# Performance work log

Hardware: AMD Instinct MI355X
Metric: run time of the kernel (lower is better)

The kernel has to match this reference:

```python
import jax, jax.numpy as jnp
import numpy as np

# ---- module hyper-params (match init_kwargs) ----
B, C_IN, C_OUT, K, H, W = 16, 128, 128, 3, 56, 56
M, G, STRIDE, RED = 2, 2, 1, 16
R = max(RED, C_IN // RED)            # GC_Attention bottleneck width = 16
MO = M * C_OUT                       # gc_att output channels
GROUPS = G * C_OUT                   # grouped 1x1 fc groups = 256
IN_PG = MO // GROUPS                 # in channels per group = M // G = 1
COUT_FC = C_OUT * C_IN * K * K       # generated weight elements per sample
OUT_PG = COUT_FC // GROUPS           # out channels per group = 576
PAD = K // 2
LN_EPS = 1e-5


def setup_inputs() -> dict:
    key = jax.random.key(0)
    ks = jax.random.split(key, 6)
    sc = 0.05
    return {
        "x": jax.random.normal(ks[0], (B, C_IN, H, W), jnp.float32),
        # GC_Attention: conv_mask (1x1, C->1)
        "w_mask": jax.random.normal(ks[1], (C_IN,), jnp.float32) * sc,
        "b_mask": jnp.zeros((), jnp.float32),
        # transform: conv1x1 C->R, LayerNorm(R), ReLU, conv1x1 R->M*out
        "w1": jax.random.normal(ks[2], (R, C_IN), jnp.float32) * sc,
        "b1": jnp.zeros((R,), jnp.float32),
        "ln_g": jnp.ones((R,), jnp.float32),
        "ln_b": jnp.zeros((R,), jnp.float32),
        "w2": jax.random.normal(ks[3], (MO, R), jnp.float32) * sc,
        "b2": jnp.zeros((MO,), jnp.float32),
        # fc: grouped 1x1 conv, groups=G*out, stored [groups, out_pg, in_pg]
        "w_fc": jax.random.normal(ks[4], (GROUPS, OUT_PG, IN_PG), jnp.float32) * sc,
        "b_fc": jnp.zeros((COUT_FC,), jnp.float32),
    }


def reference(x, w_mask, b_mask, w1, b1, ln_g, ln_b, w2, b2, w_fc, b_fc):
    b, c, h, w = x.shape
    # --- GC_Attention: global-context pooling via spatial softmax ---
    mask = jnp.einsum('bchw,c->bhw', x, w_mask) + b_mask        # [b,h,w]
    att = jax.nn.softmax(mask.reshape(b, -1), axis=-1)          # [b,hw]
    ctx = jnp.einsum('bcs,bs->bc', x.reshape(b, c, -1), att)    # [b,C]
    # bottleneck transform (1x1 convs on [b,*,1,1] == dense layers)
    t = ctx @ w1.T + b1                                          # [b,R]
    mu = t.mean(-1, keepdims=True)
    var = t.var(-1, keepdims=True)
    t = (t - mu) / jnp.sqrt(var + LN_EPS) * ln_g + ln_b          # LayerNorm over R
    t = jax.nn.relu(t)
    a = jax.nn.sigmoid(t @ w2.T + b2)                            # [b, M*out]
    # --- grouped 1x1 conv: generate per-sample conv weights ---
    xw = jnp.einsum('bgi,goi->bgo', a.reshape(b, GROUPS, IN_PG), w_fc)
    xw = xw.reshape(b, COUT_FC) + b_fc
    Wd = xw.reshape(b, C_OUT, C_IN, K, K)                        # per-sample kernels
    # --- per-sample conv2d (torch: groups=b on batch-folded input) ---
    def conv1(xi, wi):
        return jax.lax.conv_general_dilated(
            xi[None], wi, (STRIDE, STRIDE), [(PAD, PAD), (PAD, PAD)],
            dimension_numbers=('NCHW', 'OIHW', 'NCHW'))[0]
    return jax.vmap(conv1)(x, Wd)                                # [b, out, H, W]
```

## Files before the change

### kernel.cpp

```cpp
#include <hip/hip_runtime.h>
#include <hip/hip_bf16.h>
#include <math.h>

#define BATCH 16
#define CIN   128
#define COUT  128
#define SS    3136
#define KKTOT 1152
#define XT_ROW 8192
#define XT_PER_B (58*XT_ROW)
#define NKB   18

typedef __attribute__((ext_vector_type(8))) __bf16 bf16x8;
typedef __attribute__((ext_vector_type(4))) float  floatx4;

static __device__ __forceinline__ unsigned short f2bf(float f) {
  union { float f; unsigned u; } v; v.f = f;
  unsigned r = v.u + 0x7fffu + ((v.u >> 16) & 1u);
  return (unsigned short)(r >> 16);
}
static __device__ __forceinline__ float bf2f(unsigned short u) {
  union { unsigned u; float f; } v; v.u = ((unsigned)u) << 16; return v.f;
}

static __device__ __forceinline__ float waveReduceSum(float v) {
  #pragma unroll
  for (int off = 32; off > 0; off >>= 1) v += __shfl_xor(v, off, 64);
  return v;
}
static __device__ __forceinline__ float waveReduceMax(float v) {
  #pragma unroll
  for (int off = 32; off > 0; off >>= 1) v = fmaxf(v, __shfl_xor(v, off, 64));
  return v;
}

static __device__ __forceinline__ void load_lds16(const void* g, void* l) {
  __builtin_amdgcn_global_load_lds(
      (const __attribute__((address_space(1))) void*)g,
      (__attribute__((address_space(3))) void*)l, 16, 0, 0);
}

__global__ void k0_padT(const float* __restrict__ x, const float* __restrict__ w_mask,
                        const float* __restrict__ b_mask,
                        unsigned short* __restrict__ xT, float* __restrict__ att) {
  int b = blockIdx.y, prow = blockIdx.x, t = threadIdx.x;
  int y = prow - 1;
  __shared__ unsigned short sx[128 * 58];
  __shared__ float swm[128];
  __shared__ float red[4 * 56];
  bool rowvalid = ((unsigned)y < 56u);
  if (t < 128) swm[t] = w_mask[t];
  if (rowvalid) {
    int ci = t >> 1, h = t & 1;
    const float* src = x + (size_t)(b * 128 + ci) * SS + y * 56 + h * 28;
    #pragma unroll
    for (int c = 0; c < 28; c++) sx[ci * 58 + h * 28 + c] = f2bf(src[c]);
  } else {
    for (int i = t; i < 128 * 58; i += 256) sx[i] = 0;
  }
  __syncthreads();
  if (rowvalid && t < 224) {
    int xx = t % 56, g = t / 56;
    float acc = 0.f;
    #pragma unroll
    for (int k = 0; k < 32; k++) {
      int ci = g * 32 + k;
      acc += bf2f(sx[ci * 58 + xx]) * swm[ci];
    }
    red[g * 56 + xx] = acc;
  }
  __syncthreads();
  if (rowvalid && t < 56)
    att[b * SS + y * 56 + t] = red[t] + red[56 + t] + red[112 + t] + red[168 + t] + b_mask[0];
  int pcol = t >> 2, cig = t & 3;
  int xx = pcol - 1;
  bool colv = rowvalid && ((unsigned)xx < 56u);
  unsigned short tmp[32];
  #pragma unroll
  for (int i = 0; i < 32; i++)
    tmp[i] = colv ? sx[(cig * 32 + i) * 58 + xx] : (unsigned short)0;
  unsigned short* dst = xT + ((size_t)(b * 58 + prow) * 64 + pcol) * 128 + cig * 32;
  #pragma unroll
  for (int q = 0; q < 4; q++)
    *reinterpret_cast<uint4*>(dst + q * 8) = *reinterpret_cast<const uint4*>(tmp + q * 8);
}

__global__ void k2_softmax(float* __restrict__ att, float* __restrict__ zinv) {
  int b = blockIdx.x, t = threadIdx.x;
  float* ab = att + b * SS;
  __shared__ float red[16];
  float m = -1e30f;
  for (int i = t; i < SS; i += 1024) m = fmaxf(m, ab[i]);
  m = waveReduceMax(m);
  if ((t & 63) == 0) red[t >> 6] = m;
  __syncthreads();
  float M = red[0];
  #pragma unroll
  for (int i = 1; i < 16; i++) M = fmaxf(M, red[i]);
  __syncthreads();
  float sum = 0.f;
  for (int i = t; i < SS; i += 1024) { float e = expf(ab[i] - M); ab[i] = e; sum += e; }
  sum = waveReduceSum(sum);
  if ((t & 63) == 0) red[t >> 6] = sum;
  __syncthreads();
  if (t == 0) {
    float S = 0.f;
    #pragma unroll
    for (int i = 0; i < 16; i++) S += red[i];
    zinv[b] = 1.0f / S;
  }
}

__global__ void k3_ctx(const float* __restrict__ x, const float* __restrict__ att,
                       const float* __restrict__ zinv, float* __restrict__ ctx) {
  int c = blockIdx.x, b = blockIdx.y, t = threadIdx.x;
  const float4* xb = (const float4*)(x + ((size_t)b * CIN + c) * SS);
  const float4* ab = (const float4*)(att + b * SS);
  float acc = 0.f;
  for (int i = t; i < 784; i += 256) {
    float4 xv = xb[i], av = ab[i];
    acc += xv.x * av.x + xv.y * av.y + xv.z * av.z + xv.w * av.w;
  }
  __shared__ float red[4];
  acc = waveReduceSum(acc);
  if ((t & 63) == 0) red[t >> 6] = acc;
  __syncthreads();
  if (t == 0) ctx[b * CIN + c] = (red[0] + red[1] + red[2] + red[3]) * zinv[b];
}

__global__ void k4_transform(const float* __restrict__ ctx, const float* __restrict__ w1,
                             const float* __restrict__ b1, const float* __restrict__ ln_g,
                             const float* __restrict__ ln_b, const float* __restrict__ w2,
                             const float* __restrict__ b2, float* __restrict__ aout) {
  int b = blockIdx.x, t = threadIdx.x;
  __shared__ float sc[128], st[16], sn[16];
  sc[t] = ctx[b * 128 + t];
  sc[t + 64] = ctx[b * 128 + t + 64];
  __syncthreads();
  if (t < 16) {
    float acc = b1[t];
    #pragma unroll 8
    for (int c = 0; c < 128; c++) acc += sc[c] * w1[t * 128 + c];
    st[t] = acc;
  }
  __syncthreads();
  float mu = 0.f, m2 = 0.f;
  #pragma unroll
  for (int r = 0; r < 16; r++) { mu += st[r]; m2 += st[r] * st[r]; }
  mu *= (1.f / 16.f); m2 *= (1.f / 16.f);
  float rstd = rsqrtf(m2 - mu * mu + 1e-5f);
  if (t < 16) {
    float v = (st[t] - mu) * rstd * ln_g[t] + ln_b[t];
    sn[t] = fmaxf(v, 0.f);
  }
  __syncthreads();
  #pragma unroll
  for (int i = 0; i < 4; i++) {
    int mo = t + 64 * i;
    float acc = b2[mo];
    #pragma unroll
    for (int r = 0; r < 16; r++) acc += sn[r] * w2[mo * 16 + r];
    aout[b * 256 + mo] = 1.f / (1.f + expf(-acc));
  }
}

__global__ void k5_wdgen(const float* __restrict__ a, const float* __restrict__ w_fc,
                         const float* __restrict__ b_fc, unsigned short* __restrict__ wd) {
  int co = blockIdx.x, b = blockIdx.y, t = threadIdx.x;
  float a0 = a[b * 256 + 2 * co], a1 = a[b * 256 + 2 * co + 1];
  const float* wrow = w_fc + co * 1152;
  const float* brow = b_fc + co * 1152;
  unsigned short* drow = wd + (size_t)(b * 128 + co) * 1152;
  #pragma unroll
  for (int r = 0; r < 9; r++) {
    int e = t + 128 * r;
    int ci = e / 9, khw = e - (e / 9) * 9;
    float v = (ci < 64 ? a0 : a1) * wrow[e] + brow[e];
    int kb = khw * 2 + (ci >> 6);
    int kq = ci & 63;
    int pos = (((kq >> 3) ^ (co & 7)) << 3) | (kq & 7);
    drow[kb * 64 + pos] = f2bf(v);
  }
}

__global__ __launch_bounds__(512, 4) void k6_conv(const unsigned short* __restrict__ xT,
                                                  const unsigned short* __restrict__ wd,
                                                  float* __restrict__ out) {
  __shared__ __align__(16) unsigned short As[8192];
  __shared__ __align__(16) unsigned short Bs[8192];
  int t = threadIdx.x;
  int b = blockIdx.y, y0 = blockIdx.x * 2;
  int wave = t >> 6, lane = t & 63, l15 = lane & 15, quad = lane >> 4;
  int x7 = lane & 7;
  const unsigned short* wp  = wd + (size_t)b * (128 * 1152);
  const unsigned short* xTb = xT + (size_t)b * XT_PER_B;

  int ch0 = wave * 128 + lane, ch1 = ch0 + 64;
  int offA0 = (ch0 >> 3) * 1152 + (ch0 & 7) * 8;
  int offA1 = (ch1 >> 3) * 1152 + (ch1 & 7) * 8;
  int s0 = ch0 >> 3, s1 = ch1 >> 3;
  int c_ = lane & 7;
  int sr0 = s0 / 56, sc0 = s0 - sr0 * 56; if (sr0 >= 2) { sr0 = 0; sc0 = 0; }
  int sr1 = s1 / 56, sc1 = s1 - sr1 * 56; if (sr1 >= 2) { sr1 = 0; sc1 = 0; }
  int offB0 = (y0 + sr0) * XT_ROW + sc0 * 128 + (c_ ^ (s0 & 7)) * 8;
  int offB1 = (y0 + sr1) * XT_ROW + sc1 * 128 + (c_ ^ (s1 & 7)) * 8;
  unsigned short* dA0 = &As[wave * 1024];
  unsigned short* dA1 = &As[wave * 1024 + 512];
  unsigned short* dB0 = &Bs[wave * 1024];
  unsigned short* dB1 = &Bs[wave * 1024 + 512];

  int s_base = (wave & 3) * 32;
  int co_b   = (wave >> 2) * 64;

  floatx4 acc[4][2];
  floatx4 zero = {0.f, 0.f, 0.f, 0.f};
  #pragma unroll
  for (int i = 0; i < 4; i++)
    #pragma unroll
    for (int j = 0; j < 2; j++) acc[i][j] = zero;

  for (int kb = 0; kb < NKB; kb++) {
    int khw = kb >> 1;
    int kh = khw / 3;
    int kw = khw - kh * 3;
    int dB = kh * XT_ROW + kw * 128 + ((kb & 1) << 6);
    int dA = kb * 64;
    __syncthreads();
    load_lds16(wp + offA0 + dA, dA0);
    load_lds16(wp + offA1 + dA, dA1);
    load_lds16(xTb + offB0 + dB, dB0);
    load_lds16(xTb + offB1 + dB, dB1);
    __syncthreads();
    #pragma unroll
    for (int kk = 0; kk < 2; kk++) {
      bf16x8 af[4], bfr[2];
      int pc = ((kk * 4 + quad) ^ x7) << 3;
      #pragma unroll
      for (int i = 0; i < 4; i++)
        af[i] = *reinterpret_cast<const bf16x8*>(&As[(co_b + i * 16 + l15) * 64 + pc]);
      #pragma unroll
      for (int j = 0; j < 2; j++)
        bfr[j] = *reinterpret_cast<const bf16x8*>(&Bs[(s_base + j * 16 + l15) * 64 + pc]);
      #pragma unroll
      for (int i = 0; i < 4; i++)
        #pragma unroll
        for (int j = 0; j < 2; j++)
          acc[i][j] = __builtin_amdgcn_mfma_f32_16x16x32_bf16(af[i], bfr[j], acc[i][j], 0, 0, 0);
    }
  }

  float* ob = out + (size_t)b * COUT * SS + y0 * 56;
  #pragma unroll
  for (int i = 0; i < 4; i++) {
    #pragma unroll
    for (int j = 0; j < 2; j++) {
      int sl = s_base + j * 16 + l15;
      if (sl < 112) {
        int row = (sl >= 56) ? 1 : 0;
        int col = sl - row * 56;
        #pragma unroll
        for (int r = 0; r < 4; r++) {
          int co = co_b + i * 16 + quad * 4 + r;
          ob[(size_t)co * SS + row * 56 + col] = acc[i][j][r];
        }
      }
    }
  }
}

extern "C" void kernel_launch(void* const* d_in, const int* in_sizes, int n_in,
                              void* d_out, int out_size, void* d_ws, size_t ws_size,
                              hipStream_t stream) {
  const float* x      = (const float*)d_in[0];
  const float* w_mask = (const float*)d_in[1];
  const float* b_mask = (const float*)d_in[2];
  const float* w1     = (const float*)d_in[3];
  const float* b1     = (const float*)d_in[4];
  const float* ln_g   = (const float*)d_in[5];
  const float* ln_b   = (const float*)d_in[6];
  const float* w2     = (const float*)d_in[7];
  const float* b2     = (const float*)d_in[8];
  const float* w_fc   = (const float*)d_in[9];
  const float* b_fc   = (const float*)d_in[10];
  float* out = (float*)d_out;

  char* ws = (char*)d_ws;
  unsigned short* xT  = (unsigned short*)(ws);
  unsigned short* wdw = (unsigned short*)(ws + 15204352);
  float* att  = (float*)(ws + 19922944);
  float* ctx  = (float*)(ws + 20123648);
  float* aact = (float*)(ws + 20131840);
  float* zinv = (float*)(ws + 20148224);

  k0_padT     <<<dim3(58, 16),   dim3(256),  0, stream>>>(x, w_mask, b_mask, xT, att);
  k2_softmax  <<<dim3(16),       dim3(1024), 0, stream>>>(att, zinv);
  k3_ctx      <<<dim3(128, 16),  dim3(256),  0, stream>>>(x, att, zinv, ctx);
  k4_transform<<<dim3(16),       dim3(64),   0, stream>>>(ctx, w1, b1, ln_g, ln_b, w2, b2, aact);
  k5_wdgen    <<<dim3(128, 16),  dim3(128),  0, stream>>>(aact, w_fc, b_fc, wdw);
  k6_conv     <<<dim3(28, 16),   dim3(512),  0, stream>>>(xT, wdw, out);
}
```

Baseline: 142.5 us.

## Double-buffer conv LDS loads and fold softmax exp into the mask kernel

The conv kernel now uses two LDS buffers with explicit vmcnt waits, so the next K-block's global-to-LDS loads are in flight while MFMAs run on the current block, hiding load latency. Separately, the softmax kernel is removed: exp is computed directly in the padding/mask kernel and the normalizer is accumulated by atomics, dropping a launch and an extra pass over att. The exp skips max-subtraction, which risks overflow for larger logits, and doubling LDS to 64KB per block may lower occupancy.

```diff
diff --git a/kernel.cpp b/kernel.cpp
--- a/kernel.cpp
+++ b/kernel.cpp
@@ -6,7 +6,6 @@
 #define CIN   128
 #define COUT  128
 #define SS    3136
-#define KKTOT 1152
 #define XT_ROW 8192
 #define XT_PER_B (58*XT_ROW)
 #define NKB   18
@@ -28,11 +27,6 @@
   for (int off = 32; off > 0; off >>= 1) v += __shfl_xor(v, off, 64);
   return v;
 }
-static __device__ __forceinline__ float waveReduceMax(float v) {
-  #pragma unroll
-  for (int off = 32; off > 0; off >>= 1) v = fmaxf(v, __shfl_xor(v, off, 64));
-  return v;
-}
 
 static __device__ __forceinline__ void load_lds16(const void* g, void* l) {
   __builtin_amdgcn_global_load_lds(
@@ -40,9 +34,15 @@
       (__attribute__((address_space(3))) void*)l, 16, 0, 0);
 }
 
+#define ASM_WAIT_VM4   asm volatile("s_waitcnt vmcnt(4)" ::: "memory")
+#define ASM_WAIT_VM0   asm volatile("s_waitcnt vmcnt(0)" ::: "memory")
+#define ASM_WAIT_LGKM0 asm volatile("s_waitcnt lgkmcnt(0)" ::: "memory")
+#define BARRIER        __builtin_amdgcn_s_barrier()
+
 __global__ void k0_padT(const float* __restrict__ x, const float* __restrict__ w_mask,
                         const float* __restrict__ b_mask,
-                        unsigned short* __restrict__ xT, float* __restrict__ att) {
+                        unsigned short* __restrict__ xT, float* __restrict__ att,
+                        float* __restrict__ zsum) {
   int b = blockIdx.y, prow = blockIdx.x, t = threadIdx.x;
   int y = prow - 1;
   __shared__ unsigned short sx[128 * 58];
@@ -70,8 +70,16 @@
     red[g * 56 + xx] = acc;
   }
   __syncthreads();
-  if (rowvalid && t < 56)
-    att[b * SS + y * 56 + t] = red[t] + red[56 + t] + red[112 + t] + red[168 + t] + b_mask[0];
+  float e = 0.f;
+  if (rowvalid && t < 56) {
+    float m = red[t] + red[56 + t] + red[112 + t] + red[168 + t] + b_mask[0];
+    e = expf(m);
+    att[b * SS + y * 56 + t] = e;
+  }
+  if (t < 64) {
+    float s = waveReduceSum(e);
+    if (t == 0 && rowvalid) atomicAdd(zsum + b, s);
+  }
   int pcol = t >> 2, cig = t & 3;
   int xx = pcol - 1;
   bool colv = rowvalid && ((unsigned)xx < 56u);
@@ -85,34 +93,8 @@
     *reinterpret_cast<uint4*>(dst + q * 8) = *reinterpret_cast<const uint4*>(tmp + q * 8);
 }
 
-__global__ void k2_softmax(float* __restrict__ att, float* __restrict__ zinv) {
-  int b = blockIdx.x, t = threadIdx.x;
-  float* ab = att + b * SS;
-  __shared__ float red[16];
-  float m = -1e30f;
-  for (int i = t; i < SS; i += 1024) m = fmaxf(m, ab[i]);
-  m = waveReduceMax(m);
-  if ((t & 63) == 0) red[t >> 6] = m;
-  __syncthreads();
-  float M = red[0];
-  #pragma unroll
-  for (int i = 1; i < 16; i++) M = fmaxf(M, red[i]);
-  __syncthreads();
-  float sum = 0.f;
-  for (int i = t; i < SS; i += 1024) { float e = expf(ab[i] - M); ab[i] = e; sum += e; }
-  sum = waveReduceSum(sum);
-  if ((t & 63) == 0) red[t >> 6] = sum;
-  __syncthreads();
-  if (t == 0) {
-    float S = 0.f;
-    #pragma unroll
-    for (int i = 0; i < 16; i++) S += red[i];
-    zinv[b] = 1.0f / S;
-  }
-}
-
 __global__ void k3_ctx(const float* __restrict__ x, const float* __restrict__ att,
-                       const float* __restrict__ zinv, float* __restrict__ ctx) {
+                       const float* __restrict__ zsum, float* __restrict__ ctx) {
   int c = blockIdx.x, b = blockIdx.y, t = threadIdx.x;
   const float4* xb = (const float4*)(x + ((size_t)b * CIN + c) * SS);
   const float4* ab = (const float4*)(att + b * SS);
@@ -125,7 +107,7 @@
   acc = waveReduceSum(acc);
   if ((t & 63) == 0) red[t >> 6] = acc;
   __syncthreads();
-  if (t == 0) ctx[b * CIN + c] = (red[0] + red[1] + red[2] + red[3]) * zinv[b];
+  if (t == 0) ctx[b * CIN + c] = (red[0] + red[1] + red[2] + red[3]) / zsum[b];
 }
 
 __global__ void k4_transform(const float* __restrict__ ctx, const float* __restrict__ w1,
@@ -186,8 +168,8 @@
 __global__ __launch_bounds__(512, 4) void k6_conv(const unsigned short* __restrict__ xT,
                                                   const unsigned short* __restrict__ wd,
                                                   float* __restrict__ out) {
-  __shared__ __align__(16) unsigned short As[8192];
-  __shared__ __align__(16) unsigned short Bs[8192];
+  __shared__ __align__(16) unsigned short As[2][8192];
+  __shared__ __align__(16) unsigned short Bs[2][8192];
   int t = threadIdx.x;
   int b = blockIdx.y, y0 = blockIdx.x * 2;
   int wave = t >> 6, lane = t & 63, l15 = lane & 15, quad = lane >> 4;
@@ -204,10 +186,6 @@
   int sr1 = s1 / 56, sc1 = s1 - sr1 * 56; if (sr1 >= 2) { sr1 = 0; sc1 = 0; }
   int offB0 = (y0 + sr0) * XT_ROW + sc0 * 128 + (c_ ^ (s0 & 7)) * 8;
   int offB1 = (y0 + sr1) * XT_ROW + sc1 * 128 + (c_ ^ (s1 & 7)) * 8;
-  unsigned short* dA0 = &As[wave * 1024];
-  unsigned short* dA1 = &As[wave * 1024 + 512];
-  unsigned short* dB0 = &Bs[wave * 1024];
-  unsigned short* dB1 = &Bs[wave * 1024 + 512];
 
   int s_base = (wave & 3) * 32;
   int co_b   = (wave >> 2) * 64;
@@ -219,35 +197,61 @@
     #pragma unroll
     for (int j = 0; j < 2; j++) acc[i][j] = zero;
 
-  for (int kb = 0; kb < NKB; kb++) {
-    int khw = kb >> 1;
-    int kh = khw / 3;
-    int kw = khw - kh * 3;
-    int dB = kh * XT_ROW + kw * 128 + ((kb & 1) << 6);
-    int dA = kb * 64;
-    __syncthreads();
-    load_lds16(wp + offA0 + dA, dA0);
-    load_lds16(wp + offA1 + dA, dA1);
-    load_lds16(xTb + offB0 + dB, dB0);
-    load_lds16(xTb + offB1 + dB, dB1);
-    __syncthreads();
-    #pragma unroll
-    for (int kk = 0; kk < 2; kk++) {
-      bf16x8 af[4], bfr[2];
-      int pc = ((kk * 4 + quad) ^ x7) << 3;
-      #pragma unroll
-      for (int i = 0; i < 4; i++)
-        af[i] = *reinterpret_cast<const bf16x8*>(&As[(co_b + i * 16 + l15) * 64 + pc]);
-      #pragma unroll
-      for (int j = 0; j < 2; j++)
-        bfr[j] = *reinterpret_cast<const bf16x8*>(&Bs[(s_base + j * 16 + l15) * 64 + pc]);
-      #pragma unroll
-      for (int i = 0; i < 4; i++)
-        #pragma unroll
-        for (int j = 0; j < 2; j++)
-          acc[i][j] = __builtin_amdgcn_mfma_f32_16x16x32_bf16(af[i], bfr[j], acc[i][j], 0, 0, 0);
-    }
-  }
+#define ISSUE(KB, P) do {                                             \
+    int khw_ = (KB) >> 1; int kh_ = khw_ / 3;                          \
+    int kw_ = khw_ - kh_ * 3;                                          \
+    int dB_ = kh_ * XT_ROW + kw_ * 128 + (((KB) & 1) << 6);            \
+    int dA_ = (KB) * 64;                                               \
+    load_lds16(wp + offA0 + dA_, &As[P][wave * 1024]);                 \
+    load_lds16(wp + offA1 + dA_, &As[P][wave * 1024 + 512]);           \
+    load_lds16(xTb + offB0 + dB_, &Bs[P][wave * 1024]);                \
+    load_lds16(xTb + offB1 + dB_, &Bs[P][wave * 1024 + 512]);          \
+  } while (0)
+
+#define COMPUTE(P) do {                                                           \
+    _Pragma("unroll")                                                             \
+    for (int kk = 0; kk < 2; kk++) {                                              \
+      bf16x8 af[4], bfr[2];                                                       \
+      int pc = ((kk * 4 + quad) ^ x7) << 3;                                       \
+      _Pragma("unroll")                                                           \
+      for (int i = 0; i < 4; i++)                                                 \
+        af[i] = *reinterpret_cast<const bf16x8*>(&As[P][(co_b + i * 16 + l15) * 64 + pc]); \
+      _Pragma("unroll")                                                           \
+      for (int j = 0; j < 2; j++)                                                 \
+        bfr[j] = *reinterpret_cast<const bf16x8*>(&Bs[P][(s_base + j * 16 + l15) * 64 + pc]); \
+      _Pragma("unroll")                                                           \
+      for (int i = 0; i < 4; i++)                                                 \
+        _Pragma("unroll")                                                         \
+        for (int j = 0; j < 2; j++)                                               \
+          acc[i][j] = __builtin_amdgcn_mfma_f32_16x16x32_bf16(af[i], bfr[j], acc[i][j], 0, 0, 0); \
+    }                                                                             \
+  } while (0)
+
+  ISSUE(0, 0);
+  ISSUE(1, 1);
+  #pragma unroll 1
+  for (int kb = 0; kb < 16; kb += 2) {
+    ASM_WAIT_VM4;
+    BARRIER;
+    COMPUTE(0);
+    ASM_WAIT_LGKM0;
+    BARRIER;
+    ISSUE(kb + 2, 0);
+    ASM_WAIT_VM4;
+    BARRIER;
+    COMPUTE(1);
+    ASM_WAIT_LGKM0;
+    BARRIER;
+    ISSUE(kb + 3, 1);
+  }
+  ASM_WAIT_VM4;
+  BARRIER;
+  COMPUTE(0);
+  ASM_WAIT_VM0;
+  BARRIER;
+  COMPUTE(1);
+#undef ISSUE
+#undef COMPUTE
 
   float* ob = out + (size_t)b * COUT * SS + y0 * 56;
   #pragma unroll
@@ -290,11 +294,11 @@
   float* att  = (float*)(ws + 19922944);
   float* ctx  = (float*)(ws + 20123648);
   float* aact = (float*)(ws + 20131840);
-  float* zinv = (float*)(ws + 20148224);
-
-  k0_padT     <<<dim3(58, 16),   dim3(256),  0, stream>>>(x, w_mask, b_mask, xT, att);
-  k2_softmax  <<<dim3(16),       dim3(1024), 0, stream>>>(att, zinv);
-  k3_ctx      <<<dim3(128, 16),  dim3(256),  0, stream>>>(x, att, zinv, ctx);
+  float* zsum = (float*)(ws + 20148224);
+
+  hipMemsetAsync(zsum, 0, 64, stream);
+  k0_padT     <<<dim3(58, 16),   dim3(256),  0, stream>>>(x, w_mask, b_mask, xT, att, zsum);
+  k3_ctx      <<<dim3(128, 16),  dim3(256),  0, stream>>>(x, att, zsum, ctx);
   k4_transform<<<dim3(16),       dim3(64),   0, stream>>>(ctx, w1, b1, ln_g, ln_b, w2, b2, aact);
   k5_wdgen    <<<dim3(128, 16),  dim3(128),  0, stream>>>(aact, w_fc, b_fc, wdw);
   k6_conv     <<<dim3(28, 16),   dim3(512),  0, stream>>>(xT, wdw, out);
```

After: 145.8 us. +2.3%, slower.

## Fuse softmax-context pooling into pad kernel and merge transform into weight generation

Applied to the files above, without the earlier changes.

The spatial softmax and context pooling are folded into the padding/transpose kernel: each row block computes exp of the mask logits, a row sum, and per-channel partial context sums from the bf16 tile already in shared memory. The bottleneck transform is merged into the weight-generation kernel, with each block recomputing the small MLP for its sample. This removes three kernel launches and a second full read of x. In exchange the max-subtraction is dropped from the softmax, which risks overflow for large logits, context now uses bf16-rounded x, and the transform is redundantly recomputed across 128 blocks per sample.

```diff
diff --git a/kernel.cpp b/kernel.cpp
--- a/kernel.cpp
+++ b/kernel.cpp
@@ -6,7 +6,6 @@
 #define CIN   128
 #define COUT  128
 #define SS    3136
-#define KKTOT 1152
 #define XT_ROW 8192
 #define XT_PER_B (58*XT_ROW)
 #define NKB   18
@@ -28,11 +27,6 @@
   for (int off = 32; off > 0; off >>= 1) v += __shfl_xor(v, off, 64);
   return v;
 }
-static __device__ __forceinline__ float waveReduceMax(float v) {
-  #pragma unroll
-  for (int off = 32; off > 0; off >>= 1) v = fmaxf(v, __shfl_xor(v, off, 64));
-  return v;
-}
 
 static __device__ __forceinline__ void load_lds16(const void* g, void* l) {
   __builtin_amdgcn_global_load_lds(
@@ -42,12 +36,14 @@
 
 __global__ void k0_padT(const float* __restrict__ x, const float* __restrict__ w_mask,
                         const float* __restrict__ b_mask,
-                        unsigned short* __restrict__ xT, float* __restrict__ att) {
+                        unsigned short* __restrict__ xT, float* __restrict__ rowsum,
+                        float* __restrict__ pctx) {
   int b = blockIdx.y, prow = blockIdx.x, t = threadIdx.x;
   int y = prow - 1;
   __shared__ unsigned short sx[128 * 58];
   __shared__ float swm[128];
   __shared__ float red[4 * 56];
+  __shared__ float se[56];
   bool rowvalid = ((unsigned)y < 56u);
   if (t < 128) swm[t] = w_mask[t];
   if (rowvalid) {
@@ -70,8 +66,28 @@
     red[g * 56 + xx] = acc;
   }
   __syncthreads();
-  if (rowvalid && t < 56)
-    att[b * SS + y * 56 + t] = red[t] + red[56 + t] + red[112 + t] + red[168 + t] + b_mask[0];
+  float e = 0.f;
+  if (rowvalid && t < 56) {
+    float m = red[t] + red[56 + t] + red[112 + t] + red[168 + t] + b_mask[0];
+    e = expf(m);
+    se[t] = e;
+  }
+  if (t < 64) {
+    float s = waveReduceSum(e);
+    if (t == 0) rowsum[b * 58 + prow] = s;
+  }
+  __syncthreads();
+  {
+    int c = t >> 1, h = t & 1;
+    float acc = 0.f;
+    if (rowvalid) {
+      #pragma unroll
+      for (int j = 0; j < 28; j++)
+        acc += bf2f(sx[c * 58 + h * 28 + j]) * se[h * 28 + j];
+    }
+    acc += __shfl_xor(acc, 1, 64);
+    if (h == 0) pctx[(size_t)(b * 58 + prow) * 128 + c] = acc;
+  }
   int pcol = t >> 2, cig = t & 3;
   int xx = pcol - 1;
   bool colv = rowvalid && ((unsigned)xx < 56u);
@@ -85,68 +101,35 @@
     *reinterpret_cast<uint4*>(dst + q * 8) = *reinterpret_cast<const uint4*>(tmp + q * 8);
 }
 
-__global__ void k2_softmax(float* __restrict__ att, float* __restrict__ zinv) {
-  int b = blockIdx.x, t = threadIdx.x;
-  float* ab = att + b * SS;
-  __shared__ float red[16];
-  float m = -1e30f;
-  for (int i = t; i < SS; i += 1024) m = fmaxf(m, ab[i]);
-  m = waveReduceMax(m);
-  if ((t & 63) == 0) red[t >> 6] = m;
-  __syncthreads();
-  float M = red[0];
-  #pragma unroll
-  for (int i = 1; i < 16; i++) M = fmaxf(M, red[i]);
-  __syncthreads();
-  float sum = 0.f;
-  for (int i = t; i < SS; i += 1024) { float e = expf(ab[i] - M); ab[i] = e; sum += e; }
-  sum = waveReduceSum(sum);
-  if ((t & 63) == 0) red[t >> 6] = sum;
-  __syncthreads();
-  if (t == 0) {
-    float S = 0.f;
-    #pragma unroll
-    for (int i = 0; i < 16; i++) S += red[i];
-    zinv[b] = 1.0f / S;
-  }
-}
-
-__global__ void k3_ctx(const float* __restrict__ x, const float* __restrict__ att,
-                       const float* __restrict__ zinv, float* __restrict__ ctx) {
-  int c = blockIdx.x, b = blockIdx.y, t = threadIdx.x;
-  const float4* xb = (const float4*)(x + ((size_t)b * CIN + c) * SS);
-  const float4* ab = (const float4*)(att + b * SS);
+__global__ void k5_gen(const float* __restrict__ rowsum, const float* __restrict__ pctx,
+                       const float* __restrict__ w1, const float* __restrict__ b1,
+                       const float* __restrict__ ln_g, const float* __restrict__ ln_b,
+                       const float* __restrict__ w2, const float* __restrict__ b2,
+                       const float* __restrict__ w_fc, const float* __restrict__ b_fc,
+                       unsigned short* __restrict__ wd) {
+  int co = blockIdx.x, b = blockIdx.y, t = threadIdx.x;
+  __shared__ float sc[128], st[16], sn[16], sa[2], shz;
+  float rv = (t < 58) ? rowsum[b * 58 + t] : 0.f;
   float acc = 0.f;
-  for (int i = t; i < 784; i += 256) {
-    float4 xv = xb[i], av = ab[i];
-    acc += xv.x * av.x + xv.y * av.y + xv.z * av.z + xv.w * av.w;
-  }
-  __shared__ float red[4];
-  acc = waveReduceSum(acc);
-  if ((t & 63) == 0) red[t >> 6] = acc;
-  __syncthreads();
-  if (t == 0) ctx[b * CIN + c] = (red[0] + red[1] + red[2] + red[3]) * zinv[b];
-}
-
-__global__ void k4_transform(const float* __restrict__ ctx, const float* __restrict__ w1,
-                             const float* __restrict__ b1, const float* __restrict__ ln_g,
-                             const float* __restrict__ ln_b, const float* __restrict__ w2,
-                             const float* __restrict__ b2, float* __restrict__ aout) {
-  int b = blockIdx.x, t = threadIdx.x;
-  __shared__ float sc[128], st[16], sn[16];
-  sc[t] = ctx[b * 128 + t];
-  sc[t + 64] = ctx[b * 128 + t + 64];
+  #pragma unroll
+  for (int r = 0; r < 58; r++) acc += pctx[(size_t)(b * 58 + r) * 128 + t];
+  if (t < 64) {
+    float z = waveReduceSum(rv);
+    if (t == 0) shz = 1.0f / z;
+  }
+  __syncthreads();
+  sc[t] = acc * shz;
   __syncthreads();
   if (t < 16) {
-    float acc = b1[t];
+    float s = b1[t];
     #pragma unroll 8
-    for (int c = 0; c < 128; c++) acc += sc[c] * w1[t * 128 + c];
-    st[t] = acc;
+    for (int c = 0; c < 128; c++) s += sc[c] * w1[t * 128 + c];
+    st[t] = s;
   }
   __syncthreads();
   float mu = 0.f, m2 = 0.f;
   #pragma unroll
-  for (int r = 0; r < 16; r++) { mu += st[r]; m2 += st[r] * st[r]; }
+  for (int r = 0; r < 16; r++) { float v = st[r]; mu += v; m2 += v * v; }
   mu *= (1.f / 16.f); m2 *= (1.f / 16.f);
   float rstd = rsqrtf(m2 - mu * mu + 1e-5f);
   if (t < 16) {
@@ -154,20 +137,15 @@
     sn[t] = fmaxf(v, 0.f);
   }
   __syncthreads();
-  #pragma unroll
-  for (int i = 0; i < 4; i++) {
-    int mo = t + 64 * i;
-    float acc = b2[mo];
-    #pragma unroll
-    for (int r = 0; r < 16; r++) acc += sn[r] * w2[mo * 16 + r];
-    aout[b * 256 + mo] = 1.f / (1.f + expf(-acc));
-  }
-}
-
-__global__ void k5_wdgen(const float* __restrict__ a, const float* __restrict__ w_fc,
-                         const float* __restrict__ b_fc, unsigned short* __restrict__ wd) {
-  int co = blockIdx.x, b = blockIdx.y, t = threadIdx.x;
-  float a0 = a[b * 256 + 2 * co], a1 = a[b * 256 + 2 * co + 1];
+  if (t < 2) {
+    int mo = 2 * co + t;
+    float s = b2[mo];
+    #pragma unroll
+    for (int r = 0; r < 16; r++) s += sn[r] * w2[mo * 16 + r];
+    sa[t] = 1.f / (1.f + expf(-s));
+  }
+  __syncthreads();
+  float a0 = sa[0], a1 = sa[1];
   const float* wrow = w_fc + co * 1152;
   const float* brow = b_fc + co * 1152;
   unsigned short* drow = wd + (size_t)(b * 128 + co) * 1152;
@@ -287,15 +265,11 @@
   char* ws = (char*)d_ws;
   unsigned short* xT  = (unsigned short*)(ws);
   unsigned short* wdw = (unsigned short*)(ws + 15204352);
-  float* att  = (float*)(ws + 19922944);
-  float* ctx  = (float*)(ws + 20123648);
-  float* aact = (float*)(ws + 20131840);
-  float* zinv = (float*)(ws + 20148224);
-
-  k0_padT     <<<dim3(58, 16),   dim3(256),  0, stream>>>(x, w_mask, b_mask, xT, att);
-  k2_softmax  <<<dim3(16),       dim3(1024), 0, stream>>>(att, zinv);
-  k3_ctx      <<<dim3(128, 16),  dim3(256),  0, stream>>>(x, att, zinv, ctx);
-  k4_transform<<<dim3(16),       dim3(64),   0, stream>>>(ctx, w1, b1, ln_g, ln_b, w2, b2, aact);
-  k5_wdgen    <<<dim3(128, 16),  dim3(128),  0, stream>>>(aact, w_fc, b_fc, wdw);
-  k6_conv     <<<dim3(28, 16),   dim3(512),  0, stream>>>(xT, wdw, out);
-}
+  float* rowsum = (float*)(ws + 19922944);
+  float* pctx   = (float*)(ws + 19927040);
+
+  k0_padT<<<dim3(58, 16),  dim3(256), 0, stream>>>(x, w_mask, b_mask, xT, rowsum, pctx);
+  k5_gen <<<dim3(128, 16), dim3(128), 0, stream>>>(rowsum, pctx, w1, b1, ln_g, ln_b,
+                                                   w2, b2, w_fc, b_fc, wdw);
+  k6_conv<<<dim3(28, 16),  dim3(512), 0, stream>>>(xT, wdw, out);
+}
```

Result: faster. 134.0 us (-6.0%).
